# Performance work log

Hardware: AMD Instinct MI355X
Metric: run time of the kernel (lower is better)

The kernel has to match this reference:

```python
import jax, jax.numpy as jnp
import numpy as np

N_EMBDS = 1024
N_HEADS = 16
HEAD_DIM = N_EMBDS // N_HEADS


def setup_inputs() -> dict:
    key = jax.random.key(0)
    ks = jax.random.split(key, 5)
    B, T, C = 2, 2048, N_EMBDS
    x = jax.random.normal(ks[0], (B, T, C), dtype=jnp.float32)
    s = 1.0 / np.sqrt(C)
    W_attn = jax.random.normal(ks[1], (C, 3 * C), dtype=jnp.float32) * s
    b_attn = jnp.zeros((3 * C,), dtype=jnp.float32)
    W_proj = jax.random.normal(ks[2], (C, C), dtype=jnp.float32) * s
    b_proj = jnp.zeros((C,), dtype=jnp.float32)
    return {"x": x, "W_attn": W_attn, "b_attn": b_attn, "W_proj": W_proj, "b_proj": b_proj}


def reference(x, W_attn, b_attn, W_proj, b_proj):
    B, T, C = x.shape
    H, D = N_HEADS, HEAD_DIM
    qkv = x @ W_attn + b_attn  # [B, T, 3C]
    q, k, v = jnp.split(qkv, 3, axis=-1)
    # [B, H, T, D]
    q = q.reshape(B, T, H, D).transpose(0, 2, 1, 3)
    k = k.reshape(B, T, H, D).transpose(0, 2, 1, 3)
    v = v.reshape(B, T, H, D).transpose(0, 2, 1, 3)
    att = jnp.einsum('bhqd,bhkd->bhqk', q, k) * (1.0 / np.sqrt(D))  # [B,H,T,T]
    causal = jnp.tril(jnp.ones((T, T), dtype=bool))
    att = jnp.where(causal[None, None], att, -jnp.inf)
    att = jax.nn.softmax(att, axis=-1)
    y = jnp.einsum('bhqk,bhkd->bhqd', att, v)  # [B,H,T,D]
    y = y.transpose(0, 2, 1, 3).reshape(B, T, C)
    return y @ W_proj + b_proj
```

## Files before the change

### kernel.cpp

```cpp
#include <hip/hip_runtime.h>
#include <hip/hip_bf16.h>


typedef __bf16 bf16x8 __attribute__((ext_vector_type(8)));
typedef float  f32x4  __attribute__((ext_vector_type(4)));
#define BF16 __hip_bfloat16

constexpr int Bb = 2, Tt = 2048, Cc = 1024, Hh = 16, Dd = 64;
constexpr float NEG_INF = -1e30f;

__device__ __forceinline__ f32x4 mfma16(bf16x8 a, bf16x8 b, f32x4 c) {
  return __builtin_amdgcn_mfma_f32_16x16x32_bf16(a, b, c, 0, 0, 0);
}

__device__ __forceinline__ void gll16(const void* g, void* l) {
  __builtin_amdgcn_global_load_lds((const __attribute__((address_space(1))) void*)g,
                                   (__attribute__((address_space(3))) void*)l,
                                   16, 0, 0);
}

__device__ __forceinline__ int swz64(int r, int c) {
  return r * 64 + ((((c >> 3) ^ r) & 7) << 3) + (c & 7);
}

__device__ __forceinline__ int kperm(int kr) {
  return (((kr >> 5) << 1) + ((kr >> 2) & 1)) * 16 + (((kr >> 3) & 3) << 2) + (kr & 3);
}

__global__ void prep_kernel(const float* __restrict__ x, BF16* __restrict__ xb,
                            const float* __restrict__ Wa, BF16* __restrict__ WaT,
                            const float* __restrict__ Wp, BF16* __restrict__ WpT) {
  __shared__ float tile[32][33];
  const int bx = blockIdx.x, tid = threadIdx.x;
  if (bx < 2048) {
    const int i = (bx * 256 + tid) * 8;
    const float4 a = *(const float4*)&x[i];
    const float4 b = *(const float4*)&x[i + 4];
    BF16 o[8];
    o[0] = __float2bfloat16(a.x); o[1] = __float2bfloat16(a.y);
    o[2] = __float2bfloat16(a.z); o[3] = __float2bfloat16(a.w);
    o[4] = __float2bfloat16(b.x); o[5] = __float2bfloat16(b.y);
    o[6] = __float2bfloat16(b.z); o[7] = __float2bfloat16(b.w);
    *(uint4*)&xb[i] = *(const uint4*)o;
    return;
  }
  const float* in; BF16* outT; int K, N, gx, gy;
  if (bx < 5120) {
    const int idx = bx - 2048;
    in = Wa; outT = WaT; K = 1024; N = 3072; gx = idx % 96; gy = idx / 96;
  } else {
    const int idx = bx - 5120;
    in = Wp; outT = WpT; K = 1024; N = 1024; gx = idx % 32; gy = idx / 32;
  }
  const int n0 = gx * 32, k0 = gy * 32;
  const int tx = tid & 31, ty = tid >> 5;
#pragma unroll
  for (int i = ty; i < 32; i += 8) tile[i][tx] = in[(size_t)(k0 + i) * N + (n0 + tx)];
  __syncthreads();
#pragma unroll
  for (int i = ty; i < 32; i += 8)
    outT[(size_t)(n0 + i) * K + (k0 + tx)] = __float2bfloat16(tile[tx][i]);
}

__global__ void transpose_v(const BF16* __restrict__ in, BF16* __restrict__ out) {
  __shared__ BF16 tile[32][33];
  const int t0 = blockIdx.x * 32, d0 = blockIdx.y * 32, bh = blockIdx.z;
  const BF16* src = in + (size_t)bh * Tt * Dd;
  BF16* dst = out + (size_t)bh * Tt * Dd;
  const int tx = threadIdx.x, ty = threadIdx.y;
#pragma unroll
  for (int i = ty; i < 32; i += 8) tile[i][tx] = src[(size_t)(t0 + i) * Dd + (d0 + tx)];
  __syncthreads();
#pragma unroll
  for (int i = ty; i < 32; i += 8) dst[(size_t)(d0 + i) * Tt + (t0 + tx)] = tile[tx][i];
}

template <int MODE>
__global__ __launch_bounds__(256) void gemm_bt(const BF16* __restrict__ A,
                                               const BF16* __restrict__ Bt,
                                               const float* __restrict__ bias,
                                               BF16* __restrict__ oq,
                                               BF16* __restrict__ ok,
                                               BF16* __restrict__ ov,
                                               float* __restrict__ fout,
                                               int Ndim, int Kdim) {
  __shared__ alignas(16) BF16 sA[128 * 32];
  __shared__ alignas(16) BF16 sB[128 * 32];
  const int tid = threadIdx.x;
  const int wave = tid >> 6, lane = tid & 63;
  const int quad = lane >> 4, l16 = lane & 15;
  const int wm = (wave >> 1) * 64, wn = (wave & 1) * 64;
  const int bm = blockIdx.y * 128, bn = blockIdx.x * 128;

  f32x4 acc[4][4];
#pragma unroll
  for (int i = 0; i < 4; ++i)
#pragma unroll
    for (int j = 0; j < 4; ++j) acc[i][j] = f32x4{0.f, 0.f, 0.f, 0.f};

  const int rowA = wave * 32 + (lane >> 2);
  const int sub8 = (lane & 3) * 8;
  const BF16* gA0 = &A[(size_t)(bm + rowA) * Kdim + sub8];
  const BF16* gB0 = &Bt[(size_t)(bn + rowA) * Kdim + sub8];
  const size_t rstep16 = (size_t)16 * Kdim;
  BF16* lA0 = &sA[wave * 1024];
  BF16* lA1 = &sA[wave * 1024 + 512];
  BF16* lB0 = &sB[wave * 1024];
  BF16* lB1 = &sB[wave * 1024 + 512];

  for (int k0 = 0; k0 < Kdim; k0 += 32) {
    __syncthreads();
    gll16(gA0 + k0, lA0);
    gll16(gA0 + rstep16 + k0, lA1);
    gll16(gB0 + k0, lB0);
    gll16(gB0 + rstep16 + k0, lB1);
    __syncthreads();

    bf16x8 af[4], bf_[4];
#pragma unroll
    for (int i = 0; i < 4; ++i)
      af[i] = *(const bf16x8*)&sA[(wm + i * 16 + l16) * 32 + quad * 8];
#pragma unroll
    for (int j = 0; j < 4; ++j)
      bf_[j] = *(const bf16x8*)&sB[(wn + j * 16 + l16) * 32 + quad * 8];
#pragma unroll
    for (int i = 0; i < 4; ++i)
#pragma unroll
      for (int j = 0; j < 4; ++j) acc[i][j] = mfma16(af[i], bf_[j], acc[i][j]);
  }

#pragma unroll
  for (int j = 0; j < 4; ++j) {
    const int gn = bn + wn + j * 16 + l16;
    const float bsv = bias[gn];
#pragma unroll
    for (int i = 0; i < 4; ++i) {
#pragma unroll
      for (int r = 0; r < 4; ++r) {
        const int gm = bm + wm + i * 16 + quad * 4 + r;
        float val = acc[i][j][r] + bsv;
        if (MODE == 0) {
          const int which = gn >> 10, c = gn & 1023;
          const int hh = c >> 6, dd = c & 63;
          const int bb = gm >> 11, tk = gm & 2047;
          if (which == 0) val *= 0.125f;
          BF16* dst = (which == 0) ? oq : (which == 1) ? ok : ov;
          dst[(((size_t)(bb * Hh + hh)) * Tt + tk) * Dd + dd] = __float2bfloat16(val);
        } else {
          fout[(size_t)gm * Ndim + gn] = val;
        }
      }
    }
  }
}

__global__ __launch_bounds__(256) void attn_kernel(const BF16* __restrict__ qg,
                                                   const BF16* __restrict__ kg,
                                                   const BF16* __restrict__ vtg,
                                                   BF16* __restrict__ yb) {
  __shared__ alignas(16) BF16 sK[64 * 64];
  __shared__ alignas(16) BF16 sV[64 * 64];
  const int pr = blockIdx.x, h = blockIdx.y, b = blockIdx.z;
  const int tid = threadIdx.x;
  const int wave = tid >> 6, lane = tid & 63;
  const int quad = lane >> 4, l16 = lane & 15;
  const int qs = (wave >> 1) ? (63 - pr) : pr;
  const int sub = wave & 1;
  const int jt_diag = qs >> 1;
  const int jt_max = (63 - pr) >> 1;
  const size_t base = ((size_t)(b * Hh + h)) * Tt * Dd;
  const int qrow0 = qs * 32 + sub * 16;

  bf16x8 qf0, qf1;
  {
    const size_t off = base + (size_t)(qrow0 + l16) * Dd;
    qf0 = *(const bf16x8*)&qg[off + quad * 8];
    qf1 = *(const bf16x8*)&qg[off + 32 + quad * 8];
  }

  bf16x8 ones8;
#pragma unroll
  for (int j = 0; j < 8; ++j) ones8[j] = (__bf16)1.0f;

  f32x4 o[4], oL;
#pragma unroll
  for (int i = 0; i < 4; ++i) o[i] = f32x4{0.f, 0.f, 0.f, 0.f};
  oL = f32x4{0.f, 0.f, 0.f, 0.f};

  const int krow = tid >> 2, kcg = (tid & 3) * 16;
  const int kprow = kperm(krow);

  uint4 rk0, rk1, rv0, rv1;
  {
    const uint4* pk = (const uint4*)&kg[base + (size_t)krow * Dd + kcg];
    const uint4* pv = (const uint4*)&vtg[base + (size_t)krow * Tt + kcg];
    rk0 = pk[0]; rk1 = pk[1];
    rv0 = pv[0]; rv1 = pv[1];
  }

  for (int jt = 0; jt <= jt_max; ++jt) {
    __syncthreads();
    *(uint4*)&sK[swz64(kprow, kcg)]     = rk0;
    *(uint4*)&sK[swz64(kprow, kcg + 8)] = rk1;
    *(uint4*)&sV[swz64(krow, kcg)]      = rv0;
    *(uint4*)&sV[swz64(krow, kcg + 8)]  = rv1;
    if (jt < jt_max) {
      const int kb2 = (jt + 1) * 64;
      const uint4* nk = (const uint4*)&kg[base + (size_t)(kb2 + krow) * Dd + kcg];
      const uint4* nv = (const uint4*)&vtg[base + (size_t)krow * Tt + kb2 + kcg];
      rk0 = nk[0]; rk1 = nk[1];
      rv0 = nv[0]; rv1 = nv[1];
    }
    __syncthreads();

    if (jt > jt_diag) continue;
    const int kb = jt * 64;

    f32x4 sS[4];
#pragma unroll
    for (int t = 0; t < 4; ++t) {
      const bf16x8 kf0 = *(const bf16x8*)&sK[swz64(t * 16 + l16, quad * 8)];
      const bf16x8 kf1 = *(const bf16x8*)&sK[swz64(t * 16 + l16, 32 + quad * 8)];
      sS[t] = mfma16(kf0, qf0, f32x4{0.f, 0.f, 0.f, 0.f});
      sS[t] = mfma16(kf1, qf1, sS[t]);
    }

    if (jt == jt_diag) {
      const int q = qrow0 + l16;
#pragma unroll
      for (int t = 0; t < 4; ++t) {
        const int kc0 = kb + (t >> 1) * 32 + quad * 8 + (t & 1) * 4;
#pragma unroll
        for (int r = 0; r < 4; ++r)
          if (kc0 + r > q) sS[t][r] = NEG_INF;
      }
    }

    bf16x8 pf[2];
#pragma unroll
    for (int cc = 0; cc < 2; ++cc)
#pragma unroll
      for (int j = 0; j < 8; ++j)
        pf[cc][j] = (__bf16)__expf(sS[cc * 2 + (j >> 2)][j & 3] - 12.0f);

#pragma unroll
    for (int cc = 0; cc < 2; ++cc) {
#pragma unroll
      for (int dt = 0; dt < 4; ++dt) {
        const bf16x8 vb =
            *(const bf16x8*)&sV[swz64(dt * 16 + l16, cc * 32 + quad * 8)];
        o[dt] = mfma16(pf[cc], vb, o[dt]);
      }
      oL = mfma16(pf[cc], ones8, oL);
    }
  }

#pragma unroll
  for (int r = 0; r < 4; ++r) {
    const float inv = 1.0f / oL[r];
    const int trow = qrow0 + quad * 4 + r;
#pragma unroll
    for (int dt = 0; dt < 4; ++dt)
      yb[((size_t)(b * Tt + trow)) * Cc + h * Dd + dt * 16 + l16] =
          __float2bfloat16(o[dt][r] * inv);
  }
}

extern "C" void kernel_launch(void* const* d_in, const int* in_sizes, int n_in,
                              void* d_out, int out_size, void* d_ws, size_t ws_size,
                              hipStream_t stream) {
  (void)in_sizes; (void)n_in; (void)out_size; (void)ws_size;
  const float* x      = (const float*)d_in[0];
  const float* W_attn = (const float*)d_in[1];
  const float* b_attn = (const float*)d_in[2];
  const float* W_proj = (const float*)d_in[3];
  const float* b_proj = (const float*)d_in[4];
  float* out = (float*)d_out;

  constexpr size_t SZ_WA = (size_t)3072 * 1024;
  constexpr size_t SZ_WP = (size_t)1024 * 1024;
  constexpr size_t SZ_X  = (size_t)4096 * 1024;
  constexpr size_t SZ_T  = (size_t)Bb * Hh * Tt * Dd;

  BF16* ws   = (BF16*)d_ws;
  BF16* wtAb = ws;
  BF16* wtPb = wtAb + SZ_WA;
  BF16* xb   = wtPb + SZ_WP;
  BF16* q    = xb + SZ_X;
  BF16* k    = q + SZ_T;
  BF16* v    = k + SZ_T;
  BF16* vt   = v + SZ_T;
  BF16* yb   = vt + SZ_T;

  prep_kernel<<<dim3(6144), 256, 0, stream>>>(x, xb, W_attn, wtAb, W_proj, wtPb);
  gemm_bt<0><<<dim3(24, 32), 256, 0, stream>>>(xb, wtAb, b_attn, q, k, v, nullptr,
                                               3072, 1024);
  transpose_v<<<dim3(64, 2, 32), dim3(32, 8), 0, stream>>>(v, vt);
  attn_kernel<<<dim3(32, 16, 2), 256, 0, stream>>>(q, k, vt, yb);
  gemm_bt<1><<<dim3(8, 32), 256, 0, stream>>>(yb, wtPb, b_proj, nullptr, nullptr,
                                              nullptr, out, 1024, 1024);
}
```

Measured before the change: 193.4 us.

## Give each attention wave 32 query rows to reuse K/V fragments

Each wave of the attention kernel now handles two 16-row query sub-tiles (32 rows), and each block covers two 64-row strips instead of two 32-row strips. The grid is halved to match. Every K and V fragment read from LDS now feeds two MFMAs, which halves LDS traffic per FLOP and the number of K/V tile loads overall. The cost is more registers per wave (double the accumulators and Q fragments) and only 512 blocks, which lowers occupancy and parallelism on the GPU.

After: 204.6 us. 1.06x slower.

```diff
diff --git a/kernel.cpp b/kernel.cpp
--- a/kernel.cpp
+++ b/kernel.cpp
@@ -164,28 +164,31 @@
   const int tid = threadIdx.x;
   const int wave = tid >> 6, lane = tid & 63;
   const int quad = lane >> 4, l16 = lane & 15;
-  const int qs = (wave >> 1) ? (63 - pr) : pr;
-  const int sub = wave & 1;
-  const int jt_diag = qs >> 1;
-  const int jt_max = (63 - pr) >> 1;
+  const int strip = (wave >> 1) ? (31 - pr) : pr;
+  const int jt_diag = strip;
+  const int jt_max = 31 - pr;
   const size_t base = ((size_t)(b * Hh + h)) * Tt * Dd;
-  const int qrow0 = qs * 32 + sub * 16;
-
-  bf16x8 qf0, qf1;
-  {
-    const size_t off = base + (size_t)(qrow0 + l16) * Dd;
-    qf0 = *(const bf16x8*)&qg[off + quad * 8];
-    qf1 = *(const bf16x8*)&qg[off + 32 + quad * 8];
+  const int qrow0 = strip * 64 + (wave & 1) * 32;
+
+  bf16x8 qf[2][2];
+#pragma unroll
+  for (int hf = 0; hf < 2; ++hf) {
+    const size_t off = base + (size_t)(qrow0 + hf * 16 + l16) * Dd;
+    qf[hf][0] = *(const bf16x8*)&qg[off + quad * 8];
+    qf[hf][1] = *(const bf16x8*)&qg[off + 32 + quad * 8];
   }
 
   bf16x8 ones8;
 #pragma unroll
   for (int j = 0; j < 8; ++j) ones8[j] = (__bf16)1.0f;
 
-  f32x4 o[4], oL;
-#pragma unroll
-  for (int i = 0; i < 4; ++i) o[i] = f32x4{0.f, 0.f, 0.f, 0.f};
-  oL = f32x4{0.f, 0.f, 0.f, 0.f};
+  f32x4 o[2][4], oL[2];
+#pragma unroll
+  for (int hf = 0; hf < 2; ++hf) {
+#pragma unroll
+    for (int i = 0; i < 4; ++i) o[hf][i] = f32x4{0.f, 0.f, 0.f, 0.f};
+    oL[hf] = f32x4{0.f, 0.f, 0.f, 0.f};
+  }
 
   const int krow = tid >> 2, kcg = (tid & 3) * 16;
   const int kprow = kperm(krow);
@@ -216,32 +219,36 @@
     if (jt > jt_diag) continue;
     const int kb = jt * 64;
 
-    f32x4 sS[4];
+    f32x4 sS[2][4];
 #pragma unroll
     for (int t = 0; t < 4; ++t) {
       const bf16x8 kf0 = *(const bf16x8*)&sK[swz64(t * 16 + l16, quad * 8)];
       const bf16x8 kf1 = *(const bf16x8*)&sK[swz64(t * 16 + l16, 32 + quad * 8)];
-      sS[t] = mfma16(kf0, qf0, f32x4{0.f, 0.f, 0.f, 0.f});
-      sS[t] = mfma16(kf1, qf1, sS[t]);
-    }
-
-    if (jt == jt_diag) {
-      const int q = qrow0 + l16;
-#pragma unroll
-      for (int t = 0; t < 4; ++t) {
-        const int kc0 = kb + (t >> 1) * 32 + quad * 8 + (t & 1) * 4;
-#pragma unroll
-        for (int r = 0; r < 4; ++r)
-          if (kc0 + r > q) sS[t][r] = NEG_INF;
+      sS[0][t] = mfma16(kf0, qf[0][0], f32x4{0.f, 0.f, 0.f, 0.f});
+      sS[0][t] = mfma16(kf1, qf[0][1], sS[0][t]);
+      sS[1][t] = mfma16(kf0, qf[1][0], f32x4{0.f, 0.f, 0.f, 0.f});
+      sS[1][t] = mfma16(kf1, qf[1][1], sS[1][t]);
+    }
+
+    bf16x8 pf[2][2];
+#pragma unroll
+    for (int hf = 0; hf < 2; ++hf) {
+      if (jt == jt_diag) {
+        const int q = qrow0 + hf * 16 + l16;
+#pragma unroll
+        for (int t = 0; t < 4; ++t) {
+          const int kc0 = kb + (t >> 1) * 32 + quad * 8 + (t & 1) * 4;
+#pragma unroll
+          for (int r = 0; r < 4; ++r)
+            if (kc0 + r > q) sS[hf][t][r] = NEG_INF;
+        }
       }
-    }
-
-    bf16x8 pf[2];
-#pragma unroll
-    for (int cc = 0; cc < 2; ++cc)
-#pragma unroll
-      for (int j = 0; j < 8; ++j)
-        pf[cc][j] = (__bf16)__expf(sS[cc * 2 + (j >> 2)][j & 3] - 12.0f);
+#pragma unroll
+      for (int cc = 0; cc < 2; ++cc)
+#pragma unroll
+        for (int j = 0; j < 8; ++j)
+          pf[hf][cc][j] = (__bf16)__expf(sS[hf][cc * 2 + (j >> 2)][j & 3] - 12.0f);
+    }
 
 #pragma unroll
     for (int cc = 0; cc < 2; ++cc) {
@@ -249,20 +256,25 @@
       for (int dt = 0; dt < 4; ++dt) {
         const bf16x8 vb =
             *(const bf16x8*)&sV[swz64(dt * 16 + l16, cc * 32 + quad * 8)];
-        o[dt] = mfma16(pf[cc], vb, o[dt]);
+        o[0][dt] = mfma16(pf[0][cc], vb, o[0][dt]);
+        o[1][dt] = mfma16(pf[1][cc], vb, o[1][dt]);
       }
-      oL = mfma16(pf[cc], ones8, oL);
-    }
-  }
-
-#pragma unroll
-  for (int r = 0; r < 4; ++r) {
-    const float inv = 1.0f / oL[r];
-    const int trow = qrow0 + quad * 4 + r;
-#pragma unroll
-    for (int dt = 0; dt < 4; ++dt)
-      yb[((size_t)(b * Tt + trow)) * Cc + h * Dd + dt * 16 + l16] =
-          __float2bfloat16(o[dt][r] * inv);
+      oL[0] = mfma16(pf[0][cc], ones8, oL[0]);
+      oL[1] = mfma16(pf[1][cc], ones8, oL[1]);
+    }
+  }
+
+#pragma unroll
+  for (int hf = 0; hf < 2; ++hf) {
+#pragma unroll
+    for (int r = 0; r < 4; ++r) {
+      const float inv = 1.0f / oL[hf][r];
+      const int trow = qrow0 + hf * 16 + quad * 4 + r;
+#pragma unroll
+      for (int dt = 0; dt < 4; ++dt)
+        yb[((size_t)(b * Tt + trow)) * Cc + h * Dd + dt * 16 + l16] =
+            __float2bfloat16(o[hf][dt][r] * inv);
+    }
   }
 }
 
@@ -296,7 +308,7 @@
   gemm_bt<0><<<dim3(24, 32), 256, 0, stream>>>(xb, wtAb, b_attn, q, k, v, nullptr,
                                                3072, 1024);
   transpose_v<<<dim3(64, 2, 32), dim3(32, 8), 0, stream>>>(v, vt);
-  attn_kernel<<<dim3(32, 16, 2), 256, 0, stream>>>(q, k, vt, yb);
+  attn_kernel<<<dim3(16, 16, 2), 256, 0, stream>>>(q, k, vt, yb);
   gemm_bt<1><<<dim3(8, 32), 256, 0, stream>>>(yb, wtPb, b_proj, nullptr, nullptr,
                                               nullptr, out, 1024, 1024);
 }
```
